# Kernel optimization log

Measured on AMD Instinct MI355X. Metric: run time of the kernel, lower is better.

The kernel has to match this reference:

```python
import jax, jax.numpy as jnp
import numpy as np

EPS = 1e-5
PROJ_EPS = 1e-5
MAX_TANH_ARG = 15.0
NUM_LAYERS = 2

def _norm(x):
    return jnp.sqrt(jnp.sum(x * x, axis=-1, keepdims=True))

def log_map_zero(y):
    # Poincare ball log map at the origin: arctanh(||y||) * y / ||y||
    n = _norm(y)
    n_c = jnp.clip(n, EPS, 1.0 - PROJ_EPS)
    return jnp.arctanh(n_c) * y / jnp.maximum(n, EPS)

def exp_map_zero(v):
    # Poincare ball exp map at the origin: tanh(||v||) * v / ||v||
    n = _norm(v)
    n_c = jnp.clip(n, EPS, MAX_TANH_ARG)
    return jnp.tanh(n_c) * v / jnp.maximum(n, EPS)

def setup_inputs() -> dict:
    key = jax.random.key(0)
    k1, k2, k3, k4 = jax.random.split(key, 4)
    N, K, D = 50000, 32, 128
    # scale initial features so they lie inside the unit ball
    node_repr = jax.random.normal(k1, (N, D), dtype=jnp.float32) * 0.01
    adj_mat = jax.random.randint(k2, (N, K), 0, N, dtype=jnp.int32)
    weight = jax.random.uniform(k3, (N, K), dtype=jnp.float32)
    mask = jnp.ones((N, 1), dtype=jnp.float32)
    # learned params: one [D, D] matrix per layer (tie_weight=False, poincare)
    msg_weights = jax.random.normal(k4, (NUM_LAYERS, D, D), dtype=jnp.float32) * (1.0 / np.sqrt(D))
    return {"node_repr": node_repr, "adj_mat": adj_mat, "weight": weight,
            "mask": mask, "msg_weights": msg_weights}

def reference(node_repr, adj_mat, weight, mask, msg_weights):
    x = node_repr
    for step in range(NUM_LAYERS):
        # log map back to tangent space at origin (identity on first layer)
        x = (log_map_zero(x) if step > 0 else x) * mask
        msg = (x @ msg_weights[step]) * mask            # [N, D] dense projection
        nbr = msg[adj_mat]                              # [N, K, D] gather by adjacency
        combined = jnp.einsum('nk,nkd->nd', weight, nbr) * mask  # weighted neighbor sum (dropout p=0)
        x = exp_map_zero(combined) * mask               # back to the manifold
        x = jax.nn.relu(x) * mask                       # poincare activation
    return x
```

## Files before the change

kernel.cpp:

```cpp
#include <hip/hip_runtime.h>

#define EPS 1e-5f
#define PROJ_EPS 1e-5f
#define MAX_TANH_ARG 15.0f

typedef __bf16 bf16x8 __attribute__((ext_vector_type(8)));
typedef float f32x4 __attribute__((ext_vector_type(4)));
typedef float f32x2 __attribute__((ext_vector_type(2)));

__device__ __forceinline__ unsigned short f2bf(float f) {
  unsigned u = __builtin_bit_cast(unsigned, f);
  u += 0x7fffu + ((u >> 16) & 1u);
  return (unsigned short)(u >> 16);
}

union BF8 {
  unsigned short u[8];
  bf16x8 v;
  uint4 q;
};

__global__ void pack_w_kernel(const float* __restrict__ W,
                              unsigned short* __restrict__ wpack) {
  int tid = blockIdx.x * blockDim.x + threadIdx.x;
  if (tid >= 2 * 8 * 4 * 64) return;
  int lane = tid & 63;
  int s = (tid >> 6) & 3;
  int t = (tid >> 8) & 7;
  int layer = tid >> 11;
  int quad = lane >> 4;
  int n = t * 16 + (lane & 15);
  unsigned short* dst = wpack + ((size_t)((layer * 32 + t * 4 + s) * 64 + lane)) * 8;
  const float* src = W + (size_t)layer * 16384;
#pragma unroll
  for (int j = 0; j < 8; ++j) {
    int k = s * 32 + quad * 8 + j;
    dst[j] = f2bf(src[(size_t)k * 128 + n]);
  }
}

template <int MODE>
__global__ __launch_bounds__(256) void gemm_kernel(
    const float* __restrict__ xf, const unsigned short* __restrict__ xb,
    const float* __restrict__ rowscale, const unsigned short* __restrict__ wpack,
    unsigned short* __restrict__ msg4, int N, int planeBytes) {
  __shared__ unsigned short tile[64][136];
  const int lane = threadIdx.x & 63;
  const int wv = threadIdx.x >> 6;
  const int m = lane & 15;
  const int quad = lane >> 4;
  const int base = blockIdx.x * 64;
  const int wbase = base + wv * 16;
  const int row = wbase + m;
  const int rowc = row < N ? row : N - 1;

  f32x4 acc[8];
#pragma unroll
  for (int t = 0; t < 8; ++t) acc[t] = (f32x4){0.f, 0.f, 0.f, 0.f};

#pragma unroll
  for (int sk = 0; sk < 4; ++sk) {
    const int k0 = sk * 32 + quad * 8;
    BF8 a;
    if (MODE == 0) {
      const float4* xp = (const float4*)(xf + (size_t)rowc * 128 + k0);
      float4 p0 = xp[0], p1 = xp[1];
      a.u[0] = f2bf(p0.x); a.u[1] = f2bf(p0.y);
      a.u[2] = f2bf(p0.z); a.u[3] = f2bf(p0.w);
      a.u[4] = f2bf(p1.x); a.u[5] = f2bf(p1.y);
      a.u[6] = f2bf(p1.z); a.u[7] = f2bf(p1.w);
    } else {
      a.q = *(const uint4*)(xb + (size_t)rowc * 128 + k0);
    }
#pragma unroll
    for (int t = 0; t < 8; ++t) {
      BF8 b;
      b.q = *(const uint4*)(wpack + (size_t)((t * 4 + sk) * 64 + lane) * 8);
      acc[t] = __builtin_amdgcn_mfma_f32_16x16x32_bf16(a.v, b.v, acc[t], 0, 0, 0);
    }
  }

  float sc[4];
#pragma unroll
  for (int r = 0; r < 4; ++r) {
    int rr = wbase + quad * 4 + r;
    rr = rr < N ? rr : N - 1;
    float s = rowscale[rr];
    sc[r] = (MODE == 0) ? s * s : s;
  }
#pragma unroll
  for (int t = 0; t < 8; ++t) {
    const int c = t * 16 + m;
#pragma unroll
    for (int r = 0; r < 4; ++r) {
      tile[wv * 16 + quad * 4 + r][c] = f2bf(acc[t][r] * sc[r]);
    }
  }
  __syncthreads();

#pragma unroll
  for (int i = 0; i < 4; ++i) {
    const int flat = i * 4096 + (int)threadIdx.x * 16;
    const int r64 = flat >> 8;
    const int colb = flat & 255;
    const int grow = base + r64;
    if (grow < N) {
      const int plane = colb >> 6;
      const int within = colb & 63;
      *(uint4*)((char*)msg4 + (size_t)plane * planeBytes + (size_t)grow * 64 + within) =
          *(const uint4*)&tile[r64][colb >> 1];
    }
  }
}

template <int MODE>
__global__ __launch_bounds__(256) void gather_kernel(
    const unsigned short* __restrict__ msg4, const int* __restrict__ adj,
    const float* __restrict__ wgt, const float* __restrict__ mask,
    unsigned short* __restrict__ x1out, float* __restrict__ lsout,
    float* __restrict__ out, int N, int planeHW) {
  __shared__ unsigned long long pairs[64 * 33];
  const int t = threadIdx.x;
  const int lane = t & 63;
  const int wv = t >> 6;
  const int g = lane >> 2;
  const int sub = lane & 3;
  const int nbase = blockIdx.x * 64;

  for (int e = t; e < 64 * 32; e += 256) {
    const int node = e >> 5, k = e & 31;
    const int gn = nbase + node;
    int id = 0;
    float w = 0.f;
    if (gn < N) {
      id = adj[(size_t)gn * 32 + k];
      w = wgt[(size_t)gn * 32 + k];
    }
    pairs[node * 33 + k] = (unsigned long long)(unsigned)id |
        ((unsigned long long)__builtin_bit_cast(unsigned, w) << 32);
  }
  __syncthreads();

  const int mynode = wv * 16 + g;
  const int gnode = nbase + mynode;
  const unsigned long long* mp = pairs + mynode * 33;
  const int suboff = sub * 16;

  f32x2 acc[16];
#pragma unroll
  for (int i = 0; i < 16; ++i) acc[i] = (f32x2){0.f, 0.f};

#pragma unroll
  for (int p = 0; p < 4; ++p) {
    const char* plane = (const char*)(msg4 + (size_t)p * planeHW);
#pragma unroll 8
    for (int k = 0; k < 32; ++k) {
      const unsigned long long pk = mp[k];
      const unsigned id = (unsigned)pk;
      const float w = __builtin_bit_cast(float, (unsigned)(pk >> 32));
      const uint4 q = *(const uint4*)(plane + ((size_t)id * 64 + suboff));
      const f32x2 w2 = {w, w};
#pragma unroll
      for (int d = 0; d < 4; ++d) {
        const unsigned qd = (&q.x)[d];
        f32x2 v2;
        v2.x = __builtin_bit_cast(float, qd << 16);
        v2.y = __builtin_bit_cast(float, qd & 0xffff0000u);
        acc[p * 4 + d] = __builtin_elementwise_fma(v2, w2, acc[p * 4 + d]);
      }
    }
  }

  const int gcl = gnode < N ? gnode : N - 1;
  const float mm = mask[gcl];
  float s2 = 0.f;
#pragma unroll
  for (int i = 0; i < 16; ++i) {
    acc[i].x *= mm;
    acc[i].y *= mm;
    s2 = fmaf(acc[i].x, acc[i].x, s2);
    s2 = fmaf(acc[i].y, acc[i].y, s2);
  }
  s2 += __shfl_xor(s2, 1);
  s2 += __shfl_xor(s2, 2);
  const float nrm = sqrtf(s2);
  const float ncl = fminf(fmaxf(nrm, EPS), MAX_TANH_ARG);
  const float esc = tanhf(ncl) / fmaxf(nrm, EPS) * mm;
  float v[32];
#pragma unroll
  for (int i = 0; i < 16; ++i) {
    v[2 * i] = fmaxf(esc * acc[i].x, 0.f) * mm;
    v[2 * i + 1] = fmaxf(esc * acc[i].y, 0.f) * mm;
  }

  if (MODE == 0) {
    float r2 = 0.f;
#pragma unroll
    for (int i = 0; i < 32; ++i) r2 = fmaf(v[i], v[i], r2);
    r2 += __shfl_xor(r2, 1);
    r2 += __shfl_xor(r2, 2);
    if (gnode < N) {
#pragma unroll
      for (int p = 0; p < 4; ++p) {
        uint4 pk4;
        unsigned* pw = &pk4.x;
#pragma unroll
        for (int d = 0; d < 4; ++d)
          pw[d] = (unsigned)f2bf(v[p * 8 + d * 2]) |
                  ((unsigned)f2bf(v[p * 8 + d * 2 + 1]) << 16);
        *(uint4*)((char*)x1out + (size_t)gnode * 256 + p * 64 + suboff) = pk4;
      }
      if (sub == 0) {
        const float nr = sqrtf(r2);
        const float nc2 = fminf(fmaxf(nr, EPS), 1.0f - PROJ_EPS);
        const float ls = 0.5f * logf((1.f + nc2) / (1.f - nc2)) / fmaxf(nr, EPS);
        lsout[gnode] = ls * mm * mm;
      }
    }
  } else {
    if (gnode < N) {
#pragma unroll
      for (int p = 0; p < 4; ++p) {
        const int cb = p * 32 + sub * 8;
        *(float4*)(out + (size_t)gnode * 128 + cb) =
            make_float4(v[p * 8 + 0], v[p * 8 + 1], v[p * 8 + 2], v[p * 8 + 3]);
        *(float4*)(out + (size_t)gnode * 128 + cb + 4) =
            make_float4(v[p * 8 + 4], v[p * 8 + 5], v[p * 8 + 6], v[p * 8 + 7]);
      }
    }
  }
}

extern "C" void kernel_launch(void* const* d_in, const int* in_sizes, int n_in,
                              void* d_out, int out_size, void* d_ws, size_t ws_size,
                              hipStream_t stream) {
  const float* node = (const float*)d_in[0];
  const int* adj = (const int*)d_in[1];
  const float* wgt = (const float*)d_in[2];
  const float* mask = (const float*)d_in[3];
  const float* mw = (const float*)d_in[4];
  float* out = (float*)d_out;
  const int N = in_sizes[0] / 128;

  const int gb = (N + 63) / 64;
  const int planeBytes = gb * 64 * 64;
  const int planeHW = planeBytes / 2;

  char* ws = (char*)d_ws;
  unsigned short* wpack = (unsigned short*)ws;
  float* lsp = (float*)(ws + 65536);
  size_t ls_bytes = ((size_t)N * 4 + 255) & ~(size_t)255;
  unsigned short* msg4 = (unsigned short*)(ws + 65536 + ls_bytes);
  unsigned short* x1 = (unsigned short*)d_out;

  hipLaunchKernelGGL(pack_w_kernel, dim3(16), dim3(256), 0, stream, mw, wpack);
  hipLaunchKernelGGL((gemm_kernel<0>), dim3(gb), dim3(256), 0, stream,
                     node, (const unsigned short*)nullptr, mask, wpack, msg4, N, planeBytes);
  hipLaunchKernelGGL((gather_kernel<0>), dim3(gb), dim3(256), 0, stream,
                     msg4, adj, wgt, mask, x1, lsp, (float*)nullptr, N, planeHW);
  hipLaunchKernelGGL((gemm_kernel<1>), dim3(gb), dim3(256), 0, stream,
                     (const float*)nullptr, x1, lsp, wpack + 16384, msg4, N, planeBytes);
  hipLaunchKernelGGL((gather_kernel<1>), dim3(gb), dim3(256), 0, stream,
                     msg4, adj, wgt, mask, (unsigned short*)nullptr, (float*)nullptr, out, N, planeHW);
}
```

Baseline: 213.4 us.

## Fuse layer-1 gather with layer-2 GEMM and stage fp32 input through LDS

Merges the first gather/exp-map step with the second-layer projection into one kernel. The bf16 x1 row and its log-map scale now stay in shared memory instead of going through global memory, which removes a launch and the x1/lsout round trip. The first GEMM now stages coalesced fp32 rows in LDS, and each wave writes its own 16 rows of output. The fused kernel needs more LDS and more registers, which can lower occupancy for the latency-bound gather.

```diff
diff --git a/kernel.cpp b/kernel.cpp
--- a/kernel.cpp
+++ b/kernel.cpp
@@ -39,20 +39,31 @@
   }
 }
 
-template <int MODE>
-__global__ __launch_bounds__(256) void gemm_kernel(
-    const float* __restrict__ xf, const unsigned short* __restrict__ xb,
-    const float* __restrict__ rowscale, const unsigned short* __restrict__ wpack,
-    unsigned short* __restrict__ msg4, int N, int planeBytes) {
-  __shared__ unsigned short tile[64][136];
+__global__ __launch_bounds__(256) void gemm0_kernel(
+    const float* __restrict__ xf, const float* __restrict__ mask,
+    const unsigned short* __restrict__ wpack, unsigned short* __restrict__ msg1,
+    int N, int planeBytes) {
+  __shared__ union {
+    float xs[4][16][132];
+    unsigned short tile[64][136];
+  } sm;
   const int lane = threadIdx.x & 63;
   const int wv = threadIdx.x >> 6;
   const int m = lane & 15;
   const int quad = lane >> 4;
   const int base = blockIdx.x * 64;
   const int wbase = base + wv * 16;
-  const int row = wbase + m;
-  const int rowc = row < N ? row : N - 1;
+
+  {
+    const int r = lane >> 2;
+    const int c = (lane & 3) * 32;
+    const int gr = wbase + r;
+    const int grc = gr < N ? gr : N - 1;
+    const float4* src = (const float4*)(xf + (size_t)grc * 128 + c);
+#pragma unroll
+    for (int i = 0; i < 8; ++i) *(float4*)&sm.xs[wv][r][c + i * 4] = src[i];
+  }
+  __syncthreads();
 
   f32x4 acc[8];
 #pragma unroll
@@ -61,17 +72,13 @@
 #pragma unroll
   for (int sk = 0; sk < 4; ++sk) {
     const int k0 = sk * 32 + quad * 8;
+    const float4 p0 = *(const float4*)&sm.xs[wv][m][k0];
+    const float4 p1 = *(const float4*)&sm.xs[wv][m][k0 + 4];
     BF8 a;
-    if (MODE == 0) {
-      const float4* xp = (const float4*)(xf + (size_t)rowc * 128 + k0);
-      float4 p0 = xp[0], p1 = xp[1];
-      a.u[0] = f2bf(p0.x); a.u[1] = f2bf(p0.y);
-      a.u[2] = f2bf(p0.z); a.u[3] = f2bf(p0.w);
-      a.u[4] = f2bf(p1.x); a.u[5] = f2bf(p1.y);
-      a.u[6] = f2bf(p1.z); a.u[7] = f2bf(p1.w);
-    } else {
-      a.q = *(const uint4*)(xb + (size_t)rowc * 128 + k0);
-    }
+    a.u[0] = f2bf(p0.x); a.u[1] = f2bf(p0.y);
+    a.u[2] = f2bf(p0.z); a.u[3] = f2bf(p0.w);
+    a.u[4] = f2bf(p1.x); a.u[5] = f2bf(p1.y);
+    a.u[6] = f2bf(p1.z); a.u[7] = f2bf(p1.w);
 #pragma unroll
     for (int t = 0; t < 8; ++t) {
       BF8 b;
@@ -85,41 +92,38 @@
   for (int r = 0; r < 4; ++r) {
     int rr = wbase + quad * 4 + r;
     rr = rr < N ? rr : N - 1;
-    float s = rowscale[rr];
-    sc[r] = (MODE == 0) ? s * s : s;
-  }
+    const float s = mask[rr];
+    sc[r] = s * s;
+  }
+  __syncthreads();
+
 #pragma unroll
   for (int t = 0; t < 8; ++t) {
     const int c = t * 16 + m;
 #pragma unroll
-    for (int r = 0; r < 4; ++r) {
-      tile[wv * 16 + quad * 4 + r][c] = f2bf(acc[t][r] * sc[r]);
-    }
-  }
-  __syncthreads();
-
-#pragma unroll
-  for (int i = 0; i < 4; ++i) {
-    const int flat = i * 4096 + (int)threadIdx.x * 16;
-    const int r64 = flat >> 8;
-    const int colb = flat & 255;
-    const int grow = base + r64;
-    if (grow < N) {
-      const int plane = colb >> 6;
-      const int within = colb & 63;
-      *(uint4*)((char*)msg4 + (size_t)plane * planeBytes + (size_t)grow * 64 + within) =
-          *(const uint4*)&tile[r64][colb >> 1];
-    }
-  }
-}
-
-template <int MODE>
-__global__ __launch_bounds__(256) void gather_kernel(
-    const unsigned short* __restrict__ msg4, const int* __restrict__ adj,
+    for (int r = 0; r < 4; ++r)
+      sm.tile[wv * 16 + quad * 4 + r][c] = f2bf(acc[t][r] * sc[r]);
+  }
+  const int r16 = lane >> 2;
+  const int sub2 = lane & 3;
+  const int grow = wbase + r16;
+  if (grow < N) {
+#pragma unroll
+    for (int p = 0; p < 4; ++p) {
+      *(uint4*)((char*)msg1 + (size_t)p * planeBytes + (size_t)grow * 64 + sub2 * 16) =
+          *(const uint4*)((const char*)&sm.tile[wv * 16 + r16][0] + p * 64 + sub2 * 16);
+    }
+  }
+}
+
+__global__ __launch_bounds__(256) void fused_kernel(
+    const unsigned short* __restrict__ msg1, const int* __restrict__ adj,
     const float* __restrict__ wgt, const float* __restrict__ mask,
-    unsigned short* __restrict__ x1out, float* __restrict__ lsout,
-    float* __restrict__ out, int N, int planeHW) {
+    const unsigned short* __restrict__ wpack2, unsigned short* __restrict__ msg2,
+    int N, int planeBytes) {
   __shared__ unsigned long long pairs[64 * 33];
+  __shared__ unsigned short xtile[64][136];
+  __shared__ float lsb[64];
   const int t = threadIdx.x;
   const int lane = t & 63;
   const int wv = t >> 6;
@@ -152,7 +156,7 @@
 
 #pragma unroll
   for (int p = 0; p < 4; ++p) {
-    const char* plane = (const char*)(msg4 + (size_t)p * planeHW);
+    const char* plane = (const char*)msg1 + (size_t)p * planeBytes;
 #pragma unroll 8
     for (int k = 0; k < 32; ++k) {
       const unsigned long long pk = mp[k];
@@ -187,46 +191,160 @@
   const float ncl = fminf(fmaxf(nrm, EPS), MAX_TANH_ARG);
   const float esc = tanhf(ncl) / fmaxf(nrm, EPS) * mm;
   float v[32];
+  float r2 = 0.f;
 #pragma unroll
   for (int i = 0; i < 16; ++i) {
     v[2 * i] = fmaxf(esc * acc[i].x, 0.f) * mm;
     v[2 * i + 1] = fmaxf(esc * acc[i].y, 0.f) * mm;
-  }
-
-  if (MODE == 0) {
-    float r2 = 0.f;
-#pragma unroll
-    for (int i = 0; i < 32; ++i) r2 = fmaf(v[i], v[i], r2);
-    r2 += __shfl_xor(r2, 1);
-    r2 += __shfl_xor(r2, 2);
-    if (gnode < N) {
-#pragma unroll
-      for (int p = 0; p < 4; ++p) {
-        uint4 pk4;
-        unsigned* pw = &pk4.x;
-#pragma unroll
-        for (int d = 0; d < 4; ++d)
-          pw[d] = (unsigned)f2bf(v[p * 8 + d * 2]) |
-                  ((unsigned)f2bf(v[p * 8 + d * 2 + 1]) << 16);
-        *(uint4*)((char*)x1out + (size_t)gnode * 256 + p * 64 + suboff) = pk4;
+    r2 = fmaf(v[2 * i], v[2 * i], r2);
+    r2 = fmaf(v[2 * i + 1], v[2 * i + 1], r2);
+  }
+  r2 += __shfl_xor(r2, 1);
+  r2 += __shfl_xor(r2, 2);
+
+#pragma unroll
+  for (int p = 0; p < 4; ++p) {
+    uint4 pk4;
+    unsigned* pw = &pk4.x;
+#pragma unroll
+    for (int d = 0; d < 4; ++d)
+      pw[d] = (unsigned)f2bf(v[p * 8 + d * 2]) |
+              ((unsigned)f2bf(v[p * 8 + d * 2 + 1]) << 16);
+    *(uint4*)((char*)&xtile[mynode][0] + p * 64 + suboff) = pk4;
+  }
+  if (sub == 0) {
+    const float nr = sqrtf(r2);
+    const float nc2 = fminf(fmaxf(nr, EPS), 1.0f - PROJ_EPS);
+    const float ls = 0.5f * logf((1.f + nc2) / (1.f - nc2)) / fmaxf(nr, EPS);
+    lsb[mynode] = ls * mm * mm;
+  }
+  __syncthreads();
+
+  const int m = lane & 15;
+  const int quad = lane >> 4;
+  f32x4 accg[8];
+#pragma unroll
+  for (int tt = 0; tt < 8; ++tt) accg[tt] = (f32x4){0.f, 0.f, 0.f, 0.f};
+#pragma unroll
+  for (int sk = 0; sk < 4; ++sk) {
+    const int k0 = sk * 32 + quad * 8;
+    BF8 a;
+    a.q = *(const uint4*)((const char*)&xtile[wv * 16 + m][0] + k0 * 2);
+#pragma unroll
+    for (int tt = 0; tt < 8; ++tt) {
+      BF8 b;
+      b.q = *(const uint4*)(wpack2 + (size_t)((tt * 4 + sk) * 64 + lane) * 8);
+      accg[tt] = __builtin_amdgcn_mfma_f32_16x16x32_bf16(a.v, b.v, accg[tt], 0, 0, 0);
+    }
+  }
+  float sc[4];
+#pragma unroll
+  for (int r = 0; r < 4; ++r) sc[r] = lsb[wv * 16 + quad * 4 + r];
+#pragma unroll
+  for (int tt = 0; tt < 8; ++tt) {
+    const int c = tt * 16 + m;
+#pragma unroll
+    for (int r = 0; r < 4; ++r)
+      xtile[wv * 16 + quad * 4 + r][c] = f2bf(accg[tt][r] * sc[r]);
+  }
+  const int r16 = lane >> 2;
+  const int sub2 = lane & 3;
+  const int grow = nbase + wv * 16 + r16;
+  if (grow < N) {
+#pragma unroll
+    for (int p = 0; p < 4; ++p) {
+      *(uint4*)((char*)msg2 + (size_t)p * planeBytes + (size_t)grow * 64 + sub2 * 16) =
+          *(const uint4*)((const char*)&xtile[wv * 16 + r16][0] + p * 64 + sub2 * 16);
+    }
+  }
+}
+
+__global__ __launch_bounds__(256) void gather_out_kernel(
+    const unsigned short* __restrict__ msg2, const int* __restrict__ adj,
+    const float* __restrict__ wgt, const float* __restrict__ mask,
+    float* __restrict__ out, int N, int planeBytes) {
+  __shared__ unsigned long long pairs[64 * 33];
+  const int t = threadIdx.x;
+  const int lane = t & 63;
+  const int wv = t >> 6;
+  const int g = lane >> 2;
+  const int sub = lane & 3;
+  const int nbase = blockIdx.x * 64;
+
+  for (int e = t; e < 64 * 32; e += 256) {
+    const int node = e >> 5, k = e & 31;
+    const int gn = nbase + node;
+    int id = 0;
+    float w = 0.f;
+    if (gn < N) {
+      id = adj[(size_t)gn * 32 + k];
+      w = wgt[(size_t)gn * 32 + k];
+    }
+    pairs[node * 33 + k] = (unsigned long long)(unsigned)id |
+        ((unsigned long long)__builtin_bit_cast(unsigned, w) << 32);
+  }
+  __syncthreads();
+
+  const int mynode = wv * 16 + g;
+  const int gnode = nbase + mynode;
+  const unsigned long long* mp = pairs + mynode * 33;
+  const int suboff = sub * 16;
+
+  f32x2 acc[16];
+#pragma unroll
+  for (int i = 0; i < 16; ++i) acc[i] = (f32x2){0.f, 0.f};
+
+#pragma unroll
+  for (int p = 0; p < 4; ++p) {
+    const char* plane = (const char*)msg2 + (size_t)p * planeBytes;
+#pragma unroll 8
+    for (int k = 0; k < 32; ++k) {
+      const unsigned long long pk = mp[k];
+      const unsigned id = (unsigned)pk;
+      const float w = __builtin_bit_cast(float, (unsigned)(pk >> 32));
+      const uint4 q = *(const uint4*)(plane + ((size_t)id * 64 + suboff));
+      const f32x2 w2 = {w, w};
+#pragma unroll
+      for (int d = 0; d < 4; ++d) {
+        const unsigned qd = (&q.x)[d];
+        f32x2 v2;
+        v2.x = __builtin_bit_cast(float, qd << 16);
+        v2.y = __builtin_bit_cast(float, qd & 0xffff0000u);
+        acc[p * 4 + d] = __builtin_elementwise_fma(v2, w2, acc[p * 4 + d]);
       }
-      if (sub == 0) {
-        const float nr = sqrtf(r2);
-        const float nc2 = fminf(fmaxf(nr, EPS), 1.0f - PROJ_EPS);
-        const float ls = 0.5f * logf((1.f + nc2) / (1.f - nc2)) / fmaxf(nr, EPS);
-        lsout[gnode] = ls * mm * mm;
-      }
-    }
-  } else {
-    if (gnode < N) {
-#pragma unroll
-      for (int p = 0; p < 4; ++p) {
-        const int cb = p * 32 + sub * 8;
-        *(float4*)(out + (size_t)gnode * 128 + cb) =
-            make_float4(v[p * 8 + 0], v[p * 8 + 1], v[p * 8 + 2], v[p * 8 + 3]);
-        *(float4*)(out + (size_t)gnode * 128 + cb + 4) =
-            make_float4(v[p * 8 + 4], v[p * 8 + 5], v[p * 8 + 6], v[p * 8 + 7]);
-      }
+    }
+  }
+
+  const int gcl = gnode < N ? gnode : N - 1;
+  const float mm = mask[gcl];
+  float s2 = 0.f;
+#pragma unroll
+  for (int i = 0; i < 16; ++i) {
+    acc[i].x *= mm;
+    acc[i].y *= mm;
+    s2 = fmaf(acc[i].x, acc[i].x, s2);
+    s2 = fmaf(acc[i].y, acc[i].y, s2);
+  }
+  s2 += __shfl_xor(s2, 1);
+  s2 += __shfl_xor(s2, 2);
+  const float nrm = sqrtf(s2);
+  const float ncl = fminf(fmaxf(nrm, EPS), MAX_TANH_ARG);
+  const float esc = tanhf(ncl) / fmaxf(nrm, EPS) * mm;
+  if (gnode < N) {
+#pragma unroll
+    for (int p = 0; p < 4; ++p) {
+      float4 o0, o1;
+      o0.x = fmaxf(esc * acc[p * 4 + 0].x, 0.f) * mm;
+      o0.y = fmaxf(esc * acc[p * 4 + 0].y, 0.f) * mm;
+      o0.z = fmaxf(esc * acc[p * 4 + 1].x, 0.f) * mm;
+      o0.w = fmaxf(esc * acc[p * 4 + 1].y, 0.f) * mm;
+      o1.x = fmaxf(esc * acc[p * 4 + 2].x, 0.f) * mm;
+      o1.y = fmaxf(esc * acc[p * 4 + 2].y, 0.f) * mm;
+      o1.z = fmaxf(esc * acc[p * 4 + 3].x, 0.f) * mm;
+      o1.w = fmaxf(esc * acc[p * 4 + 3].y, 0.f) * mm;
+      const int cb = p * 32 + sub * 8;
+      *(float4*)(out + (size_t)gnode * 128 + cb) = o0;
+      *(float4*)(out + (size_t)gnode * 128 + cb + 4) = o1;
     }
   }
 }
@@ -244,22 +362,16 @@
 
   const int gb = (N + 63) / 64;
   const int planeBytes = gb * 64 * 64;
-  const int planeHW = planeBytes / 2;
-
-  char* ws = (char*)d_ws;
-  unsigned short* wpack = (unsigned short*)ws;
-  float* lsp = (float*)(ws + 65536);
-  size_t ls_bytes = ((size_t)N * 4 + 255) & ~(size_t)255;
-  unsigned short* msg4 = (unsigned short*)(ws + 65536 + ls_bytes);
-  unsigned short* x1 = (unsigned short*)d_out;
+
+  unsigned short* wpack = (unsigned short*)d_ws;
+  unsigned short* msg2 = (unsigned short*)((char*)d_ws + 65536);
+  unsigned short* msg1 = (unsigned short*)d_out;
 
   hipLaunchKernelGGL(pack_w_kernel, dim3(16), dim3(256), 0, stream, mw, wpack);
-  hipLaunchKernelGGL((gemm_kernel<0>), dim3(gb), dim3(256), 0, stream,
-                     node, (const unsigned short*)nullptr, mask, wpack, msg4, N, planeBytes);
-  hipLaunchKernelGGL((gather_kernel<0>), dim3(gb), dim3(256), 0, stream,
-                     msg4, adj, wgt, mask, x1, lsp, (float*)nullptr, N, planeHW);
-  hipLaunchKernelGGL((gemm_kernel<1>), dim3(gb), dim3(256), 0, stream,
-                     (const float*)nullptr, x1, lsp, wpack + 16384, msg4, N, planeBytes);
-  hipLaunchKernelGGL((gather_kernel<1>), dim3(gb), dim3(256), 0, stream,
-                     msg4, adj, wgt, mask, (unsigned short*)nullptr, (float*)nullptr, out, N, planeHW);
-}
+  hipLaunchKernelGGL(gemm0_kernel, dim3(gb), dim3(256), 0, stream,
+                     node, mask, wpack, msg1, N, planeBytes);
+  hipLaunchKernelGGL(fused_kernel, dim3(gb), dim3(256), 0, stream,
+                     msg1, adj, wgt, mask, wpack + 16384, msg2, N, planeBytes);
+  hipLaunchKernelGGL(gather_out_kernel, dim3(gb), dim3(256), 0, stream,
+                     msg2, adj, wgt, mask, out, N, planeBytes);
+}
```

New measurement: 204.5 us. 1.04x faster.
